# Kernel optimization log

Measured on AMD Instinct MI355X. Metric: run time of the kernel, lower is better.

The kernel has to match this reference:

```python
import jax, jax.numpy as jnp
import numpy as np

REPR_OUT = (16, 16, 16)   # multiplicities for l=0,1,2
STRIDE = 2                # GatedBlock stride with smooth_stride=True -> low-pass+stride after gate
PAD = 2                   # conv padding
C_IN = 72                 # 8*1 + 8*3 + 8*5
C_OUT_GATED = 176         # 144 fields + 32 gate scalars
KSIZE = 5


def conv3d(x, w, stride, padding):
    return jax.lax.conv_general_dilated(
        x, w, window_strides=(stride,) * 3,
        padding=[(padding, padding)] * 3,
        dimension_numbers=('NCDHW', 'OIDHW', 'NCDHW'))


def low_pass_filter(z, scale, stride):
    # gaussian blur (sigma from scale) applied depthwise, then strided -- as in se3cnn
    sigma = 0.5 * (scale ** 2 - 1) ** 0.5
    size = int(1 + 2 * 2.5 * sigma)
    if size % 2 == 0:
        size += 1
    r = np.arange(size) - size // 2
    g1 = np.exp(-r.astype(np.float64) ** 2 / (2 * sigma ** 2))
    g = g1[:, None, None] * g1[None, :, None] * g1[None, None, :]
    g = (g / g.sum()).astype(np.float32)
    B, C = z.shape[0], z.shape[1]
    zz = z.reshape(B * C, 1, *z.shape[2:])
    out = conv3d(zz, jnp.asarray(g)[None, None], stride, size // 2)
    return out.reshape(B, C, *out.shape[2:])


def gate(y, scalar_bias, gate_bias):
    # y: [B, 176, X, Y, Z]; split into 144 field channels + 32 gate scalars
    size_out = sum(mul * (2 * n + 1) for n, mul in enumerate(REPR_OUT))
    B, _, nx, ny, nz = y.shape
    g = jax.nn.sigmoid(y[:, size_out:] + gate_bias[None, :, None, None, None])
    fields = []
    begin_y, begin_g = 0, 0
    for n, mul in enumerate(REPR_OUT):
        if mul == 0:
            continue
        dim = 2 * n + 1
        fy = y[:, begin_y:begin_y + mul * dim]
        if n == 0:
            # scalar fields: bias + relu (ScalarActivation)
            fields.append(jax.nn.relu(fy + scalar_bias[None, :, None, None, None]))
        else:
            fg = g[:, begin_g:begin_g + mul]
            begin_g += mul
            f = fy.reshape(B, mul, dim, nx, ny, nz) * fg[:, :, None]  # broadcast gate over 2l+1
            fields.append(f.reshape(B, mul * dim, nx, ny, nz))
        begin_y += mul * dim
    return jnp.concatenate(fields, axis=1)  # [B, 144, X, Y, Z]


def setup_inputs() -> dict:
    key = jax.random.key(0)
    k1, k2, k3, k4 = jax.random.split(key, 4)
    fan_in = C_IN * KSIZE ** 3
    x = jax.random.normal(k1, (4, C_IN, 32, 32, 32), dtype=jnp.float32)
    W = jax.random.normal(k2, (C_OUT_GATED, C_IN, KSIZE, KSIZE, KSIZE), dtype=jnp.float32) / np.sqrt(fan_in)
    scalar_bias = jax.random.normal(k3, (REPR_OUT[0],), dtype=jnp.float32) * 0.1
    gate_bias = jax.random.normal(k4, (sum(REPR_OUT[1:]),), dtype=jnp.float32) * 0.1
    return {'x': x, 'W': W, 'scalar_bias': scalar_bias, 'gate_bias': gate_bias}


def reference(x, W, scalar_bias, gate_bias):
    y = conv3d(x, W, 1, PAD)                 # SE3 conv at stride 1 (smooth_stride)
    z = gate(y, scalar_bias, gate_bias)      # per-irrep gated nonlinearity
    z = low_pass_filter(z, STRIDE, STRIDE)   # gaussian low-pass + stride 2
    return z
```

## Files before the change

### kernel.cpp

```cpp
#include <hip/hip_runtime.h>
#include <cstdint>
#include <cstddef>

typedef short short8 __attribute__((ext_vector_type(8)));
typedef float floatx4 __attribute__((ext_vector_type(4)));
typedef unsigned short u16;

__device__ __forceinline__ u16 f2bf(float f) {
    unsigned u = __float_as_uint(f);
    u += 0x7FFFu + ((u >> 16) & 1u);
    return (u16)(u >> 16);
}
__device__ __forceinline__ float bf2f(u16 h) {
    return __uint_as_float(((unsigned)h) << 16);
}

__device__ __forceinline__ void gload_lds16(const u16* g, u16* l) {
    __builtin_amdgcn_global_load_lds(
        (const __attribute__((address_space(1))) void*)g,
        (__attribute__((address_space(3))) void*)l, 16, 0, 0);
}

__global__ __launch_bounds__(256) void k_transpose_x(const float* __restrict__ x,
                                                     u16* __restrict__ xt) {
    __shared__ float tile[72 * 33];
    const int bx = blockIdx.x;
    const int tid = threadIdx.x;
    const int b = bx >> 10, d = (bx >> 5) & 31, h = bx & 31;
    const float* src = x + (size_t)b * 72 * 32768 + d * 1024 + h * 32;
    for (int e = tid; e < 2304; e += 256) {
        int ci = e >> 5, w = e & 31;
        tile[ci * 33 + w] = src[(size_t)ci * 32768 + w];
    }
    __syncthreads();
    u16* dst = xt + (size_t)bx * 2304;
    for (int e = tid; e < 2304; e += 256) {
        int w = e / 72, ci = e - w * 72;
        dst[e] = f2bf(tile[ci * 33 + w]);
    }
}

__global__ __launch_bounds__(256) void k_prep_w(const float* __restrict__ W,
                                                u16* __restrict__ wt) {
    const int gid = blockIdx.x * 256 + threadIdx.x;
    const int frag = gid >> 6, lane = gid & 63;
    const int nb = frag % 11;
    int t = frag / 11;
    const int kb = t % 12;
    t = t / 12;
    const int kh = t % 5, kd = t / 5;
    const int n = lane & 15, q8 = (lane >> 4) * 8;
    const int co = nb * 16 + n;
    u16 v[8] __attribute__((aligned(16)));
    #pragma unroll
    for (int j = 0; j < 8; ++j) {
        int k = kb * 32 + q8 + j;
        u16 r = 0;
        if (k < 360) {
            int kw = k / 72, ci = k - kw * 72;
            r = f2bf(W[((size_t)co * 72 + ci) * 125 + kd * 25 + kh * 5 + kw]);
        }
        v[j] = r;
    }
    *(uint4*)(wt + (size_t)gid * 8) = *(const uint4*)v;
}

#define LP 2624
#define MFMA_BF16 __builtin_amdgcn_mfma_f32_16x16x32_bf16

#define STAGE_PAIR(s0_) do {                                                       \
    _Pragma("unroll")                                                              \
    for (int cc = 0; cc < 3; ++cc) {                                               \
        const int c_  = wv + cc * 8;                                               \
        const int st_ = (s0_) + (c_ >= 11 ? 1 : 0);                                \
        const int nb_ = (c_ >= 11) ? (c_ - 11) : c_;                               \
        if (c_ < 22 && st_ < 60)                                                   \
            gload_lds16(wt_kd + (size_t)st_ * 5632 + nb_ * 512 + lane * 8,         \
                        sB + (st_ & 3) * 5632 + nb_ * 512);                        \
    }                                                                              \
} while (0)

#define CSTEP(aoff_, buf_) do {                                                    \
    const u16* ap_ = sxA + (aoff_);                                                \
    short8 A0_ = *(const short8*)(ap_);                                            \
    short8 A1_ = *(const short8*)(ap_ + 1152);                                     \
    short8 A2_ = *(const short8*)(ap_ + LP);                                       \
    short8 A3_ = *(const short8*)(ap_ + LP + 1152);                                \
    const u16* bb_ = sB + (buf_) * 5632 + lane * 8;                                \
    _Pragma("unroll")                                                              \
    for (int j = 0; j < 11; ++j) {                                                 \
        short8 bv = *(const short8*)(bb_ + j * 512);                               \
        acc[0][j] = MFMA_BF16(A0_, bv, acc[0][j], 0, 0, 0);                        \
        acc[1][j] = MFMA_BF16(A1_, bv, acc[1][j], 0, 0, 0);                        \
        acc[2][j] = MFMA_BF16(A2_, bv, acc[2][j], 0, 0, 0);                        \
        acc[3][j] = MFMA_BF16(A3_, bv, acc[3][j], 0, 0, 0);                        \
    }                                                                              \
} while (0)

__global__ __launch_bounds__(512, 2) void k_conv(const u16* __restrict__ xt,
                                                 const u16* __restrict__ wt,
                                                 const float* __restrict__ scalar_bias,
                                                 const float* __restrict__ gate_bias,
                                                 u16* __restrict__ zt) {
    __shared__ __align__(16) u16 sx[20 * LP];
    __shared__ __align__(16) u16 sB[4 * 5632];
    const int bx = blockIdx.x;
    const int swz = (bx & 7) * 32 + (bx >> 3);
    const int ht = swz & 1, d = (swz >> 1) & 31, b = swz >> 6;
    const int h0 = ht * 16;
    const int tid = threadIdx.x, lane = tid & 63, wv = tid >> 6;
    const int c15 = lane & 15, q = lane >> 4;

    floatx4 acc[4][11];
    #pragma unroll
    for (int i = 0; i < 4; ++i) {
        #pragma unroll
        for (int j = 0; j < 11; ++j) acc[i][j] = (floatx4){0.f, 0.f, 0.f, 0.f};
    }

    const int laneA = c15 * 72 + q * 8;
    const u16* sxA = &sx[2 * wv * LP + laneA];

    for (int kd = 0; kd < 5; ++kd) {
        const int dp = d + kd - 2;
        if (dp < 0 || dp >= 32) continue;
        const u16* wt_kd = wt + (size_t)kd * 5 * 67584;

        __syncthreads();
        const u16* srcbase = xt + (size_t)((b * 32 + dp) * 32) * 2304;
        for (int idx = tid; idx < 20 * 328; idx += 512) {
            int r = idx / 328, c = idx - r * 328;
            int hp = h0 + r - 2;
            uint4 val = make_uint4(0u, 0u, 0u, 0u);
            if (hp >= 0 && hp < 32 && c >= 18 && c < 306)
                val = *(const uint4*)(srcbase + (size_t)hp * 2304 + (c * 8 - 144));
            *(uint4*)(&sx[r * LP + c * 8]) = val;
        }
        STAGE_PAIR(0);
        __syncthreads();

        int kh = 0, kb = 0;
        #pragma unroll 1
        for (int kp = 0; kp < 60; kp += 2) {
            if (kp) __syncthreads();
            STAGE_PAIR(kp + 2);
            const int aoff = kh * LP + kb * 32;
            CSTEP(aoff,      kp & 3);
            CSTEP(aoff + 32, (kp + 1) & 3);
            kb += 2;
            if (kb == 12) { kb = 0; ++kh; }
        }
    }

    const float sb = scalar_bias[c15];
    int   slA[9];
    float gbA[9];
    #pragma unroll
    for (int nb = 1; nb <= 8; ++nb) {
        int idx = (nb - 1) * 16 + c15;
        int mul = (nb <= 3) ? (idx / 3) : (16 + (idx - 48) / 5);
        slA[nb] = (lane & 48) | (mul & 15);
        gbA[nb] = gate_bias[mul];
    }
    #pragma unroll
    for (int mi = 0; mi < 4; ++mi) {
        const int hl = 2 * wv + (mi >> 1);
        const int wh = mi & 1;
        const size_t zrow0 = (size_t)((b * 32 + d) * 32 + (h0 + hl)) * 32;
        #pragma unroll
        for (int r = 0; r < 4; ++r) {
            const int w = wh * 16 + q * 4 + r;
            u16* zp = zt + (zrow0 + w) * 144;
            zp[c15] = f2bf(fmaxf(acc[mi][0][r] + sb, 0.f));
            const float g9v  = acc[mi][9][r];
            const float g10v = acc[mi][10][r];
            #pragma unroll
            for (int nb = 1; nb <= 8; ++nb) {
                float ys = __shfl((nb <= 3) ? g9v : g10v, slA[nb], 64);
                float g  = 1.f / (1.f + __expf(-(ys + gbA[nb])));
                zp[nb * 16 + c15] = f2bf(acc[mi][nb][r] * g);
            }
        }
    }
}

__global__ __launch_bounds__(256) void k_lowpass_wh(const u16* __restrict__ zt,
                                                    float* __restrict__ tmp) {
    const int gid = blockIdx.x * 256 + threadIdx.x;
    const int c8 = gid % 18;
    int r = gid / 18;
    const int ow = r & 15; r >>= 4;
    const int oh = r & 15; r >>= 4;
    const int d = r & 31;
    const int b = r >> 5;
    const float lw[5] = {0.03208210f, 0.23705644f, 0.46172277f, 0.23705644f, 0.03208210f};
    float a[8];
    #pragma unroll
    for (int j = 0; j < 8; ++j) a[j] = 0.f;
    const u16* zb = zt + (size_t)((b * 32 + d) * 32) * 32 * 144 + c8 * 8;
    for (int kh = 0; kh < 5; ++kh) {
        const int hz = 2 * oh + kh - 2;
        if (hz < 0 || hz >= 32) continue;
        const u16* rowp = zb + (size_t)hz * 32 * 144;
        #pragma unroll
        for (int kw = 0; kw < 5; ++kw) {
            const int wz = 2 * ow + kw - 2;
            if (wz < 0 || wz >= 32) continue;
            const float wt2 = lw[kh] * lw[kw];
            u16 v[8] __attribute__((aligned(16)));
            *(uint4*)v = *(const uint4*)(rowp + (size_t)wz * 144);
            #pragma unroll
            for (int j = 0; j < 8; ++j) a[j] += wt2 * bf2f(v[j]);
        }
    }
    float* tp = tmp + (size_t)(((b * 32 + d) * 16 + oh) * 16 + ow) * 144 + c8 * 8;
    *(float4*)(tp)     = make_float4(a[0], a[1], a[2], a[3]);
    *(float4*)(tp + 4) = make_float4(a[4], a[5], a[6], a[7]);
}

__global__ __launch_bounds__(256) void k_lowpass_d(const float* __restrict__ tmp,
                                                   float* __restrict__ out) {
    const int gid = blockIdx.x * 256 + threadIdx.x;
    const int oh = gid & 15;
    int r = gid >> 4;
    const int od = r & 15; r >>= 4;
    const int c = r % 144;
    const int b = r / 144;
    const float lw[5] = {0.03208210f, 0.23705644f, 0.46172277f, 0.23705644f, 0.03208210f};
    float a[16];
    #pragma unroll
    for (int j = 0; j < 16; ++j) a[j] = 0.f;
    for (int kd = 0; kd < 5; ++kd) {
        const int dz = 2 * od + kd - 2;
        if (dz < 0 || dz >= 32) continue;
        const float w = lw[kd];
        const float* base = tmp + (size_t)(((b * 32 + dz) * 16 + oh) * 16) * 144 + c;
        #pragma unroll
        for (int ow = 0; ow < 16; ++ow) a[ow] += w * base[(size_t)ow * 144];
    }
    float* op = out + ((size_t)(b * 144 + c) * 4096) + od * 256 + oh * 16;
    #pragma unroll
    for (int ow = 0; ow < 16; ++ow) op[ow] = a[ow];
}

extern "C" void kernel_launch(void* const* d_in, const int* in_sizes, int n_in,
                              void* d_out, int out_size, void* d_ws, size_t ws_size,
                              hipStream_t stream) {
    const float* x  = (const float*)d_in[0];
    const float* W  = (const float*)d_in[1];
    const float* sb = (const float*)d_in[2];
    const float* gb = (const float*)d_in[3];
    float* out = (float*)d_out;

    char* ws = (char*)d_ws;
    u16* xt = (u16*)(ws);
    u16* wt = (u16*)(ws + 18874368);
    u16* zt = (u16*)(ws + 22253568);
    float* tmp = (float*)(ws);

    hipLaunchKernelGGL(k_transpose_x, dim3(4096), dim3(256), 0, stream, x, xt);
    hipLaunchKernelGGL(k_prep_w,      dim3(825),  dim3(256), 0, stream, W, wt);
    hipLaunchKernelGGL(k_conv,        dim3(256),  dim3(512), 0, stream, xt, wt, sb, gb, zt);
    hipLaunchKernelGGL(k_lowpass_wh,  dim3(2304), dim3(256), 0, stream, zt, tmp);
    hipLaunchKernelGGL(k_lowpass_d,   dim3(576),  dim3(256), 0, stream, tmp, out);
}
```

Measured before the change: 532.6 us.

## Reorder separable low-pass passes: blur D,H first, then W with output writes

The separable Gaussian low-pass changes its pass order. The first pass now filters along D and H into a [b,od,oh,w,c] intermediate, and the second filters along W and writes the NCDHW output. The old second pass read the intermediate with a 144-float stride per thread and wrote 16 contiguous floats per thread. The new one reads contiguous float4 pairs, and adjacent threads write adjacent ow positions for each channel. The intermediate stays the same size, and the second pass now runs twice as many threads.

```diff
diff --git a/kernel.cpp b/kernel.cpp
--- a/kernel.cpp
+++ b/kernel.cpp
@@ -184,63 +184,67 @@
     }
 }
 
-__global__ __launch_bounds__(256) void k_lowpass_wh(const u16* __restrict__ zt,
+__global__ __launch_bounds__(256) void k_lowpass_dh(const u16* __restrict__ zt,
                                                     float* __restrict__ tmp) {
+    const int gid = blockIdx.x * 256 + threadIdx.x;
+    const int c8 = gid % 18;
+    int r = gid / 18;
+    const int w  = r & 31; r >>= 5;
+    const int oh = r & 15; r >>= 4;
+    const int od = r & 15; r >>= 4;
+    const int b  = r;
+    const float lw[5] = {0.03208210f, 0.23705644f, 0.46172277f, 0.23705644f, 0.03208210f};
+    float a[8];
+    #pragma unroll
+    for (int j = 0; j < 8; ++j) a[j] = 0.f;
+    for (int kd = 0; kd < 5; ++kd) {
+        const int dz = 2 * od + kd - 2;
+        if (dz < 0 || dz >= 32) continue;
+        for (int kh = 0; kh < 5; ++kh) {
+            const int hz = 2 * oh + kh - 2;
+            if (hz < 0 || hz >= 32) continue;
+            const float wt2 = lw[kd] * lw[kh];
+            const u16* p = zt + ((size_t)((b * 32 + dz) * 32 + hz) * 32 + w) * 144 + c8 * 8;
+            u16 v[8] __attribute__((aligned(16)));
+            *(uint4*)v = *(const uint4*)p;
+            #pragma unroll
+            for (int j = 0; j < 8; ++j) a[j] += wt2 * bf2f(v[j]);
+        }
+    }
+    float* tp = tmp + ((size_t)(((b * 16 + od) * 16 + oh) * 32) + w) * 144 + c8 * 8;
+    *(float4*)(tp)     = make_float4(a[0], a[1], a[2], a[3]);
+    *(float4*)(tp + 4) = make_float4(a[4], a[5], a[6], a[7]);
+}
+
+__global__ __launch_bounds__(256) void k_lowpass_w(const float* __restrict__ tmp,
+                                                   float* __restrict__ out) {
     const int gid = blockIdx.x * 256 + threadIdx.x;
     const int c8 = gid % 18;
     int r = gid / 18;
     const int ow = r & 15; r >>= 4;
     const int oh = r & 15; r >>= 4;
-    const int d = r & 31;
-    const int b = r >> 5;
+    const int od = r & 15; r >>= 4;
+    const int b  = r;
     const float lw[5] = {0.03208210f, 0.23705644f, 0.46172277f, 0.23705644f, 0.03208210f};
     float a[8];
     #pragma unroll
     for (int j = 0; j < 8; ++j) a[j] = 0.f;
-    const u16* zb = zt + (size_t)((b * 32 + d) * 32) * 32 * 144 + c8 * 8;
-    for (int kh = 0; kh < 5; ++kh) {
-        const int hz = 2 * oh + kh - 2;
-        if (hz < 0 || hz >= 32) continue;
-        const u16* rowp = zb + (size_t)hz * 32 * 144;
-        #pragma unroll
-        for (int kw = 0; kw < 5; ++kw) {
-            const int wz = 2 * ow + kw - 2;
-            if (wz < 0 || wz >= 32) continue;
-            const float wt2 = lw[kh] * lw[kw];
-            u16 v[8] __attribute__((aligned(16)));
-            *(uint4*)v = *(const uint4*)(rowp + (size_t)wz * 144);
-            #pragma unroll
-            for (int j = 0; j < 8; ++j) a[j] += wt2 * bf2f(v[j]);
-        }
-    }
-    float* tp = tmp + (size_t)(((b * 32 + d) * 16 + oh) * 16 + ow) * 144 + c8 * 8;
-    *(float4*)(tp)     = make_float4(a[0], a[1], a[2], a[3]);
-    *(float4*)(tp + 4) = make_float4(a[4], a[5], a[6], a[7]);
-}
-
-__global__ __launch_bounds__(256) void k_lowpass_d(const float* __restrict__ tmp,
-                                                   float* __restrict__ out) {
-    const int gid = blockIdx.x * 256 + threadIdx.x;
-    const int oh = gid & 15;
-    int r = gid >> 4;
-    const int od = r & 15; r >>= 4;
-    const int c = r % 144;
-    const int b = r / 144;
-    const float lw[5] = {0.03208210f, 0.23705644f, 0.46172277f, 0.23705644f, 0.03208210f};
-    float a[16];
-    #pragma unroll
-    for (int j = 0; j < 16; ++j) a[j] = 0.f;
-    for (int kd = 0; kd < 5; ++kd) {
-        const int dz = 2 * od + kd - 2;
-        if (dz < 0 || dz >= 32) continue;
-        const float w = lw[kd];
-        const float* base = tmp + (size_t)(((b * 32 + dz) * 16 + oh) * 16) * 144 + c;
-        #pragma unroll
-        for (int ow = 0; ow < 16; ++ow) a[ow] += w * base[(size_t)ow * 144];
-    }
-    float* op = out + ((size_t)(b * 144 + c) * 4096) + od * 256 + oh * 16;
-    #pragma unroll
-    for (int ow = 0; ow < 16; ++ow) op[ow] = a[ow];
+    const float* tb = tmp + ((size_t)(((b * 16 + od) * 16 + oh) * 32)) * 144 + c8 * 8;
+    #pragma unroll
+    for (int kw = 0; kw < 5; ++kw) {
+        const int wz = 2 * ow + kw - 2;
+        if (wz < 0 || wz >= 32) continue;
+        const float wt1 = lw[kw];
+        const float* p = tb + (size_t)wz * 144;
+        float4 v0 = *(const float4*)(p);
+        float4 v1 = *(const float4*)(p + 4);
+        a[0] += wt1 * v0.x; a[1] += wt1 * v0.y; a[2] += wt1 * v0.z; a[3] += wt1 * v0.w;
+        a[4] += wt1 * v1.x; a[5] += wt1 * v1.y; a[6] += wt1 * v1.z; a[7] += wt1 * v1.w;
+    }
+    const int c0 = c8 * 8;
+    float* op = out + ((size_t)b * 144 + c0) * 4096 + od * 256 + oh * 16 + ow;
+    #pragma unroll
+    for (int j = 0; j < 8; ++j) op[(size_t)j * 4096] = a[j];
 }
 
 extern "C" void kernel_launch(void* const* d_in, const int* in_sizes, int n_in,
@@ -261,6 +265,6 @@
     hipLaunchKernelGGL(k_transpose_x, dim3(4096), dim3(256), 0, stream, x, xt);
     hipLaunchKernelGGL(k_prep_w,      dim3(825),  dim3(256), 0, stream, W, wt);
     hipLaunchKernelGGL(k_conv,        dim3(256),  dim3(512), 0, stream, xt, wt, sb, gb, zt);
-    hipLaunchKernelGGL(k_lowpass_wh,  dim3(2304), dim3(256), 0, stream, zt, tmp);
-    hipLaunchKernelGGL(k_lowpass_d,   dim3(576),  dim3(256), 0, stream, tmp, out);
-}
+    hipLaunchKernelGGL(k_lowpass_dh,  dim3(2304), dim3(256), 0, stream, zt, tmp);
+    hipLaunchKernelGGL(k_lowpass_w,   dim3(1152), dim3(256), 0, stream, tmp, out);
+}
```

New measurement: 479.3 us. -10.0%, faster.
